# Kernel optimization log

Hardware: AMD Instinct MI355X
Metric: run time of the kernel (lower is better)

## Reference

```python
import jax, jax.numpy as jnp
import numpy as np

_Y_PERC = np.array([[0.01840373,0.58999538,0.99887572,1.35731124,1.51378647,1.59615814,1.60794642,1.59768487],[0.54538216,0.85649201,1.15733541,1.48270578,1.60280835,1.63332936,1.6204338,1.60154382],[0.97357237,1.15783744,1.37431718,1.6003753,1.66259869,1.65741183,1.62199538,1.60600917],[1.32983939,1.48646416,1.60701991,1.70982965,1.70294495,1.63899384,1.62378931,1.61771147],[1.51241334,1.61619203,1.6781811,1.69350727,1.68488638,1.62312361,1.60460837,1.59458518],[1.59135561,1.67050663,1.67614207,1.69062219,1.6559363,1.61859251,1.58166148,1.57357605],[1.62406025,1.64713876,1.63513799,1.6238076,1.6050742,1.57471174,1.5501197,1.54399399],[1.6153739,1.60502484,1.59157153,1.58655249,1.57093044,1.56278208,1.54476926,1.52678157]], dtype=np.float32)
_Y_QUANT = np.array([[16,11,10,16,24,40,51,61],[12,12,14,19,26,58,60,55],[14,13,16,24,40,57,69,56],[14,17,22,29,51,87,80,62],[18,22,37,56,68,109,103,77],[24,35,55,64,81,104,113,92],[49,64,78,87,103,121,120,101],[72,92,95,98,112,100,103,99]], dtype=np.float32)

def _dct8_ortho():
    # Orthonormal 8x8 DCT-II matrix (matches T_DCT_ORTHO up to fp32 rounding)
    n = np.arange(8, dtype=np.float64)
    T = np.cos(np.pi * (2.0 * n[None, :] + 1.0) * n[:, None] / 16.0) * np.sqrt(2.0 / 8.0)
    T[0, :] *= np.sqrt(0.5)
    return T.astype(np.float32)

def setup_inputs() -> dict:
    key = jax.random.key(0)
    k1, k2 = jax.random.split(key)
    B, C, H, W = 16, 3, 512, 512
    return {
        "input": jax.random.normal(k1, (B, C, H, W), dtype=jnp.float32),
        "target": jax.random.normal(k2, (B, C, H, W), dtype=jnp.float32),
        "transform": jnp.asarray(_dct8_ortho()),
        "weight": jnp.asarray(_Y_PERC / _Y_QUANT),
    }

def _blocks(x):
    # (B,C,H,W) -> (B,C,nblocks,8,8), same block ordering as torch
    # reshape(B,C,H,W//8,8).transpose(-2,-3).reshape(B,C,-1,8,8)
    B, C, H, W = x.shape
    return x.reshape(B, C, H, W // 8, 8).swapaxes(2, 3).reshape(B, C, -1, 8, 8)

def reference(input, target, transform, weight):
    # Transform is linear, so T@x@T' - T@y@T' == T@(x-y)@T' -- same math, fewer GEMMs.
    diff = _blocks(input) - _blocks(target)
    d = jnp.einsum('ij,bcnjk,lk->bcnil', transform, diff, transform)
    return jnp.mean(d * d * weight)
```

## Files before the change

kernel.cpp:

```cpp
#include <hip/hip_runtime.h>


#define WG 256
#define NWG 768
#define INV_N (1.0f/12582912.0f)

typedef float v4f __attribute__((ext_vector_type(4)));

__global__ __launch_bounds__(WG, 3) void spectral_partial(
    const float* __restrict__ x,
    const float* __restrict__ y,
    const float* __restrict__ Tm,
    const float* __restrict__ Wm,
    float* __restrict__ ws)
{
    const int tid = threadIdx.x;
    const int p   = blockIdx.x * WG + tid;
    const int img = p >> 12;
    const int rem = p & 4095;
    const int base = img * 262144 + (rem >> 6) * 4096 + (rem & 63) * 8;

    v4f xa[16], yb[16];
#pragma unroll
    for (int r = 0; r < 8; ++r) {
        const v4f* xp = reinterpret_cast<const v4f*>(x + base + r*512);
        const v4f* yp = reinterpret_cast<const v4f*>(y + base + r*512);
        xa[2*r]   = xp[0];
        xa[2*r+1] = xp[1];
        yb[2*r]   = yp[0];
        yb[2*r+1] = yp[1];
    }

    float tT[8][8];
#pragma unroll
    for (int i = 0; i < 8; ++i) {
        float4 t0 = reinterpret_cast<const float4*>(Tm)[2*i];
        float4 t1 = reinterpret_cast<const float4*>(Tm)[2*i+1];
        tT[i][0]=t0.x; tT[i][1]=t0.y; tT[i][2]=t0.z; tT[i][3]=t0.w;
        tT[i][4]=t1.x; tT[i][5]=t1.y; tT[i][6]=t1.z; tT[i][7]=t1.w;
    }

    float M[8][8];
#pragma unroll
    for (int r = 0; r < 8; ++r) {
        v4f a0 = xa[2*r], a1 = xa[2*r+1];
        v4f b0 = yb[2*r], b1 = yb[2*r+1];
        float row[8] = {a0.x-b0.x, a0.y-b0.y, a0.z-b0.z, a0.w-b0.w,
                        a1.x-b1.x, a1.y-b1.y, a1.z-b1.z, a1.w-b1.w};
#pragma unroll
        for (int l = 0; l < 8; ++l) {
            float acc = row[0]*tT[l][0];
#pragma unroll
            for (int j = 1; j < 8; ++j) acc += row[j]*tT[l][j];
            M[r][l] = acc;
        }
    }

    float s = 0.0f;
#pragma unroll
    for (int i = 0; i < 8; ++i) {
        float4 w0 = reinterpret_cast<const float4*>(Wm)[2*i];
        float4 w1 = reinterpret_cast<const float4*>(Wm)[2*i+1];
        float wr[8] = {w0.x,w0.y,w0.z,w0.w,w1.x,w1.y,w1.z,w1.w};
#pragma unroll
        for (int l = 0; l < 8; ++l) {
            float d = tT[i][0]*M[0][l];
#pragma unroll
            for (int r = 1; r < 8; ++r) d += tT[i][r]*M[r][l];
            s += wr[l]*d*d;
        }
    }

#pragma unroll
    for (int off = 32; off > 0; off >>= 1) s += __shfl_down(s, off, 64);
    __shared__ float wsum[WG/64];
    if ((tid & 63) == 0) wsum[tid >> 6] = s;
    __syncthreads();
    if (tid == 0) ws[blockIdx.x] = wsum[0] + wsum[1] + wsum[2] + wsum[3];
}

__global__ __launch_bounds__(256) void spectral_reduce(
    const float* __restrict__ ws, float* __restrict__ out)
{
    const int tid = threadIdx.x;
    float s = ws[tid] + ws[tid + 256] + ws[tid + 512];
#pragma unroll
    for (int off = 32; off > 0; off >>= 1) s += __shfl_down(s, off, 64);
    __shared__ float wsum[4];
    if ((tid & 63) == 0) wsum[tid >> 6] = s;
    __syncthreads();
    if (tid == 0) out[0] = (wsum[0]+wsum[1]+wsum[2]+wsum[3]) * INV_N;
}

extern "C" void kernel_launch(void* const* d_in, const int* in_sizes, int n_in,
                              void* d_out, int out_size, void* d_ws, size_t ws_size,
                              hipStream_t stream) {
    const float* x  = (const float*)d_in[0];
    const float* y  = (const float*)d_in[1];
    const float* Tm = (const float*)d_in[2];
    const float* Wm = (const float*)d_in[3];
    float* ws  = (float*)d_ws;
    float* out = (float*)d_out;

    spectral_partial<<<NWG, WG, 0, stream>>>(x, y, Tm, Wm, ws);
    spectral_reduce<<<1, 256, 0, stream>>>(ws, out);
}
```

Baseline: 24.29 us.

## Split each 8x8 block across lane pairs for coalesced row loads

Each wavefront now handles one strip of blocks, and lane pairs share each 8-wide block row. Every lane loads 16-byte chunks that are contiguous across the wavefront, and an xor-1 shuffle rebuilds the full row. Each lane computes half of the row-transform columns for two blocks. This replaces the old per-thread 32-byte strided loads with fully coalesced accesses and halves the per-thread M register footprint, at the cost of extra shuffles and selects.

```diff
diff --git a/kernel.cpp b/kernel.cpp
--- a/kernel.cpp
+++ b/kernel.cpp
@@ -7,6 +7,15 @@
 
 typedef float v4f __attribute__((ext_vector_type(4)));
 
+__device__ __forceinline__ v4f shflx1(v4f v) {
+    v4f r;
+    r.x = __shfl_xor(v.x, 1, 64);
+    r.y = __shfl_xor(v.y, 1, 64);
+    r.z = __shfl_xor(v.z, 1, 64);
+    r.w = __shfl_xor(v.w, 1, 64);
+    return r;
+}
+
 __global__ __launch_bounds__(WG, 3) void spectral_partial(
     const float* __restrict__ x,
     const float* __restrict__ y,
@@ -14,22 +23,13 @@
     const float* __restrict__ Wm,
     float* __restrict__ ws)
 {
-    const int tid = threadIdx.x;
-    const int p   = blockIdx.x * WG + tid;
-    const int img = p >> 12;
-    const int rem = p & 4095;
-    const int base = img * 262144 + (rem >> 6) * 4096 + (rem & 63) * 8;
-
-    v4f xa[16], yb[16];
-#pragma unroll
-    for (int r = 0; r < 8; ++r) {
-        const v4f* xp = reinterpret_cast<const v4f*>(x + base + r*512);
-        const v4f* yp = reinterpret_cast<const v4f*>(y + base + r*512);
-        xa[2*r]   = xp[0];
-        xa[2*r+1] = xp[1];
-        yb[2*r]   = yp[0];
-        yb[2*r+1] = yp[1];
-    }
+    const int tid  = threadIdx.x;
+    const int lane = tid & 63;
+    const int q    = lane & 1;
+    const int s    = blockIdx.x * 4 + (tid >> 6);
+    const int img  = s >> 6;
+    const int hb   = s & 63;
+    const int sbase = img * 262144 + hb * 4096;
 
     float tT[8][8];
 #pragma unroll
@@ -39,42 +39,76 @@
         tT[i][0]=t0.x; tT[i][1]=t0.y; tT[i][2]=t0.z; tT[i][3]=t0.w;
         tT[i][4]=t1.x; tT[i][5]=t1.y; tT[i][6]=t1.z; tT[i][7]=t1.w;
     }
+    float tl[4][8];
+#pragma unroll
+    for (int k = 0; k < 4; ++k) {
+        const float* tr = Tm + (4*q + k)*8;
+        float4 t0 = reinterpret_cast<const float4*>(tr)[0];
+        float4 t1 = reinterpret_cast<const float4*>(tr)[1];
+        tl[k][0]=t0.x; tl[k][1]=t0.y; tl[k][2]=t0.z; tl[k][3]=t0.w;
+        tl[k][4]=t1.x; tl[k][5]=t1.y; tl[k][6]=t1.z; tl[k][7]=t1.w;
+    }
+    v4f wv[8];
+#pragma unroll
+    for (int i = 0; i < 8; ++i)
+        wv[i] = *reinterpret_cast<const v4f*>(Wm + i*8 + 4*q);
 
-    float M[8][8];
+    float MA[8][4], MB[8][4];
 #pragma unroll
     for (int r = 0; r < 8; ++r) {
-        v4f a0 = xa[2*r], a1 = xa[2*r+1];
-        v4f b0 = yb[2*r], b1 = yb[2*r+1];
-        float row[8] = {a0.x-b0.x, a0.y-b0.y, a0.z-b0.z, a0.w-b0.w,
-                        a1.x-b1.x, a1.y-b1.y, a1.z-b1.z, a1.w-b1.w};
+        const float* rb = x + sbase + r*512;
+        const float* rc = y + sbase + r*512;
+        v4f xA = *reinterpret_cast<const v4f*>(rb + 4*lane);
+        v4f xB = *reinterpret_cast<const v4f*>(rb + 256 + 4*lane);
+        v4f yA = *reinterpret_cast<const v4f*>(rc + 4*lane);
+        v4f yB = *reinterpret_cast<const v4f*>(rc + 256 + 4*lane);
+        v4f dA = xA - yA;
+        v4f dB = xB - yB;
+        v4f pA = shflx1(dA);
+        v4f pB = shflx1(dB);
+
+        float rowA[8], rowB[8];
 #pragma unroll
-        for (int l = 0; l < 8; ++l) {
-            float acc = row[0]*tT[l][0];
+        for (int j = 0; j < 4; ++j) {
+            rowA[j]   = q ? pA[j] : dA[j];
+            rowA[4+j] = q ? dA[j] : pA[j];
+            rowB[j]   = q ? pB[j] : dB[j];
+            rowB[4+j] = q ? dB[j] : pB[j];
+        }
 #pragma unroll
-            for (int j = 1; j < 8; ++j) acc += row[j]*tT[l][j];
-            M[r][l] = acc;
+        for (int k = 0; k < 4; ++k) {
+            float aA = rowA[0]*tl[k][0];
+            float aB = rowB[0]*tl[k][0];
+#pragma unroll
+            for (int j = 1; j < 8; ++j) {
+                aA += rowA[j]*tl[k][j];
+                aB += rowB[j]*tl[k][j];
+            }
+            MA[r][k] = aA;
+            MB[r][k] = aB;
         }
     }
 
-    float s = 0.0f;
+    float acc = 0.0f;
 #pragma unroll
     for (int i = 0; i < 8; ++i) {
-        float4 w0 = reinterpret_cast<const float4*>(Wm)[2*i];
-        float4 w1 = reinterpret_cast<const float4*>(Wm)[2*i+1];
-        float wr[8] = {w0.x,w0.y,w0.z,w0.w,w1.x,w1.y,w1.z,w1.w};
 #pragma unroll
-        for (int l = 0; l < 8; ++l) {
-            float d = tT[i][0]*M[0][l];
+        for (int k = 0; k < 4; ++k) {
+            float dA = tT[i][0]*MA[0][k];
+            float dB = tT[i][0]*MB[0][k];
 #pragma unroll
-            for (int r = 1; r < 8; ++r) d += tT[i][r]*M[r][l];
-            s += wr[l]*d*d;
+            for (int r = 1; r < 8; ++r) {
+                dA += tT[i][r]*MA[r][k];
+                dB += tT[i][r]*MB[r][k];
+            }
+            acc += wv[i][k]*(dA*dA + dB*dB);
         }
     }
 
 #pragma unroll
-    for (int off = 32; off > 0; off >>= 1) s += __shfl_down(s, off, 64);
+    for (int off = 32; off > 0; off >>= 1) acc += __shfl_down(acc, off, 64);
     __shared__ float wsum[WG/64];
-    if ((tid & 63) == 0) wsum[tid >> 6] = s;
+    if ((tid & 63) == 0) wsum[tid >> 6] = acc;
     __syncthreads();
     if (tid == 0) ws[blockIdx.x] = wsum[0] + wsum[1] + wsum[2] + wsum[3];
 }
```

Result: slower. 25.17 us (+3.6%).
